# Performance work log

Measured on AMD Instinct MI355X. Metric: run time of the kernel, lower is better.

Reference implementation:

```python
import jax, jax.numpy as jnp
import numpy as np

NEG_SLOPE = 0.1
BN_EPS = 1e-5

def lrelu(z):
    return jax.nn.leaky_relu(z, NEG_SLOPE)

def conv1d(x, w, b):
    # x: [B,C,L], w: [O,I,K], 'same' padding for K=3
    y = jax.lax.conv_general_dilated(x, w, (1,), [(1, 1)], dimension_numbers=('NCH', 'OIH', 'NCH'))
    return y + b[None, :, None]

def batchnorm_train(x, g, be):
    # training-mode BatchNorm1d over (B, L) per channel; x: [B,C,L]
    m = x.mean(axis=(0, 2), keepdims=True)
    v = x.var(axis=(0, 2), keepdims=True)
    return g[None, :, None] * (x - m) * jax.lax.rsqrt(v + BN_EPS) + be[None, :, None]

def setup_inputs() -> dict:
    key = jax.random.key(0)
    ks = jax.random.split(key, 16)
    L, B, E = 100, 32, 512
    F, K, M, H, DEC = 256, 3, 128, 512, 512
    D = F + 2  # cnn feats + 2 coord dims
    s = 0.02
    inp = {
        'x': jax.random.normal(ks[0], (L, B, E), jnp.float32),
        'h': jax.random.normal(ks[1], (B, H), jnp.float32),
        'cw1': jax.random.normal(ks[2], (F, E, K), jnp.float32) * s,
        'cb1': jnp.zeros((F,), jnp.float32),
        'g1': jnp.ones((F,), jnp.float32), 'be1': jnp.zeros((F,), jnp.float32),
        'cw2': jax.random.normal(ks[3], (F, F, K), jnp.float32) * s,
        'cb2': jnp.zeros((F,), jnp.float32),
        'g2': jnp.ones((F,), jnp.float32), 'be2': jnp.zeros((F,), jnp.float32),
        'cw3': jax.random.normal(ks[4], (F, F, K), jnp.float32) * s,
        'cb3': jnp.zeros((F,), jnp.float32),
        'g3': jnp.ones((F,), jnp.float32), 'be3': jnp.zeros((F,), jnp.float32),
        'cw4': jax.random.normal(ks[5], (F, F, K), jnp.float32) * s,
        'cb4': jnp.zeros((F,), jnp.float32),
        'g4': jnp.ones((F,), jnp.float32), 'be4': jnp.zeros((F,), jnp.float32),
        'W1': jax.random.normal(ks[6], (2 * D + H, M), jnp.float32) * s,
        'b1': jnp.zeros((M,), jnp.float32),
        'W2': jax.random.normal(ks[7], (M, M), jnp.float32) * s,
        'b2': jnp.zeros((M,), jnp.float32),
        'W3': jax.random.normal(ks[8], (M, M), jnp.float32) * s,
        'b3': jnp.zeros((M,), jnp.float32),
        'W4': jax.random.normal(ks[9], (M, M), jnp.float32) * s,
        'b4': jnp.zeros((M,), jnp.float32),
        'F1': jax.random.normal(ks[10], (M, M), jnp.float32) * s,
        'fb1': jnp.zeros((M,), jnp.float32),
        'F2': jax.random.normal(ks[11], (M, DEC), jnp.float32) * s,
        'fb2': jnp.zeros((DEC,), jnp.float32),
    }
    return inp

def reference(x, h, cw1, cb1, g1, be1, cw2, cb2, g2, be2, cw3, cb3, g3, be3,
              cw4, cb4, g4, be4, W1, b1, W2, b2, W3, b3, W4, b4, F1, fb1, F2, fb2):
    # x: [L,B,E] -> [B,E,L]
    xc = jnp.transpose(x, (1, 2, 0))
    for cw, cb, g, be in ((cw1, cb1, g1, be1), (cw2, cb2, g2, be2),
                          (cw3, cb3, g3, be3), (cw4, cb4, g4, be4)):
        xc = batchnorm_train(lrelu(conv1d(xc, cw, cb)), g, be)
    xc = jnp.transpose(xc, (0, 2, 1))  # [B,L,F]
    B, L, _ = xc.shape
    # coordinate tensor: cvt_coord(i, L) = [(i/sqrt(L)-2)/2, (i%sqrt(L)-2)/2]
    i = jnp.arange(L, dtype=jnp.float32)
    sL = jnp.sqrt(jnp.float32(L))
    coord = jnp.stack([(i / sL - 2.0) / 2.0, (jnp.mod(i, sL) - 2.0) / 2.0], axis=-1)
    xf = jnp.concatenate([xc, jnp.broadcast_to(coord, (B, L, 2))], axis=-1)  # [B,L,D]
    D = xf.shape[-1]
    # pair[b,i,j] = [xf[b,j], xf[b,i], h[b]]; split W1 to avoid materializing concat
    Wa, Wb, Wc = W1[:D], W1[D:2 * D], W1[2 * D:]
    A = xf @ Wa                              # contribution of x_j, [B,L,M]
    C = xf @ Wb + (h @ Wc + b1)[:, None, :]  # contribution of x_i and h, [B,L,M]
    g = lrelu(C[:, :, None, :] + A[:, None, :, :])  # [B,L,L,M]
    g = lrelu(g @ W2 + b2)
    g = lrelu(g @ W3 + b3)
    g = lrelu(g @ W4 + b4)
    s = g.sum(axis=(1, 2))  # sum-pool over all L*L pairs -> [B,M]
    out = lrelu(lrelu(s @ F1 + fb1) @ F2 + fb2)  # [B,dec_hid]
    return out
```

## Files before the change

### kernel.cpp

```cpp
#include <hip/hip_runtime.h>
#include <hip/hip_bf16.h>
#include <stdint.h>
#include <stddef.h>

#define NEG 0.1f

typedef __attribute__((ext_vector_type(8))) short short8;
typedef __attribute__((ext_vector_type(16))) float floatx16;

__device__ __forceinline__ unsigned f2bf(float f) {
  union { float f; unsigned u; } v; v.f = f;
  unsigned r = v.u + 0x7FFFu + ((v.u >> 16) & 1u);
  return r >> 16;
}
__device__ __forceinline__ unsigned pk2bf(float a, float b) {
  __hip_bfloat162 hh = __float22bfloat162_rn(make_float2(a, b));
  union { __hip_bfloat162 h; unsigned u; } v; v.h = hh; return v.u;
}
__device__ __forceinline__ float bits2f(unsigned u) {
  union { unsigned u; float f; } v; v.u = u; return v.f;
}

__global__ void k_prep(const float* __restrict__ cw1, const float* __restrict__ cw2,
                       const float* __restrict__ cw3, const float* __restrict__ cw4,
                       unsigned short* __restrict__ wt1, unsigned short* __restrict__ wt2,
                       unsigned short* __restrict__ wt3, unsigned short* __restrict__ wt4,
                       const float* __restrict__ W1, unsigned short* __restrict__ wab,
                       const float* __restrict__ W2, const float* __restrict__ W3,
                       const float* __restrict__ W4, unsigned short* __restrict__ wmlp,
                       const float* __restrict__ h, float* __restrict__ hc) {
  __shared__ float tile[64 * 65];
  int bid = blockIdx.x, tid = threadIdx.x;
  if (bid < 1280) {
    int z = bid;
    int E; const float* cw; unsigned short* wt;
    if (z < 512) { E = 512; cw = cw1; wt = wt1; }
    else {
      int q = (z - 512) >> 8; E = 256;
      cw = (q == 0) ? cw2 : ((q == 1) ? cw3 : cw4);
      wt = (q == 0) ? wt2 : ((q == 1) ? wt3 : wt4);
      z = (z - 512) & 255;
    }
    int idx = z * 256 + tid;
    int f = idx / E, e = idx - f * E;
    const float* s = cw + (size_t)idx * 3;
    unsigned short* d = wt + (size_t)f * 3 * E + e;
    d[0] = (unsigned short)f2bf(s[0]);
    d[E] = (unsigned short)f2bf(s[1]);
    d[2 * E] = (unsigned short)f2bf(s[2]);
  } else if (bid < 1304) {
    int tw = bid - 1280;
    int half = tw / 12, rem = tw % 12, dt = rem >> 1, nt = rem & 1;
    int c = tid & 63, rq = tid >> 6;
#pragma unroll
    for (int it = 0; it < 16; ++it) {
      int r = rq + it * 4;
      int kp = dt * 64 + r;
      float v = 0.f;
      if (kp < 258) v = W1[(size_t)(half * 258 + kp) * 128 + nt * 64 + c];
      tile[r * 65 + c] = v;
    }
    __syncthreads();
#pragma unroll
    for (int it = 0; it < 16; ++it) {
      int r2 = rq + it * 4;
      wab[(size_t)(half * 128 + nt * 64 + r2) * 384 + dt * 64 + c] =
          (unsigned short)f2bf(tile[c * 65 + r2]);
    }
  } else if (bid < 1496) {
    int i2 = (bid - 1304) * 256 + tid;
    int n = i2 & 127, k = (i2 >> 7) & 127, zz = i2 >> 14;
    const float* W = (zz == 0) ? W2 : ((zz == 1) ? W3 : W4);
    float v = W[k * 128 + n];
    int w = n >> 5, l = ((k >> 3) & 1) * 32 + (n & 31), kk = k >> 4, j = k & 7;
    int i = (((zz * 4 + w) * 8 + kk) << 9) | (l << 3) | j;
    wmlp[i] = (unsigned short)f2bf(v);
  } else {
    int t = bid - 1496;
    int b = t >> 2, seg = t & 3;
    int m = tid & 127, sub = tid >> 7;
    int k0 = seg * 128 + sub * 64;
    const float* hr = h + b * 512 + k0;
    const float* Wc = W1 + (size_t)(516 + k0) * 128 + m;
    float a0 = 0.f, a1 = 0.f, a2 = 0.f, a3 = 0.f, a4 = 0.f, a5 = 0.f, a6 = 0.f, a7 = 0.f;
#pragma unroll
    for (int k = 0; k < 64; k += 8) {
      a0 += hr[k + 0] * Wc[(size_t)(k + 0) * 128];
      a1 += hr[k + 1] * Wc[(size_t)(k + 1) * 128];
      a2 += hr[k + 2] * Wc[(size_t)(k + 2) * 128];
      a3 += hr[k + 3] * Wc[(size_t)(k + 3) * 128];
      a4 += hr[k + 4] * Wc[(size_t)(k + 4) * 128];
      a5 += hr[k + 5] * Wc[(size_t)(k + 5) * 128];
      a6 += hr[k + 6] * Wc[(size_t)(k + 6) * 128];
      a7 += hr[k + 7] * Wc[(size_t)(k + 7) * 128];
    }
    float s = ((a0 + a1) + (a2 + a3)) + ((a4 + a5) + (a6 + a7));
    atomicAdd(&hc[b * 128 + m], s);
  }
}

__global__ __launch_bounds__(256, 2) void k_conv(
    const float* __restrict__ zin, const float* __restrict__ bnin,
    const float* __restrict__ gamv, const float* __restrict__ betv,
    const unsigned short* __restrict__ wt, const float* __restrict__ cb,
    float* __restrict__ zout, float* __restrict__ bnout, int E, int xmode) {
  extern __shared__ unsigned short smem[];
  const int SL = (E == 512) ? 520 : 264;
  unsigned short* slab = smem;
  unsigned short* Bs = smem + 34 * SL;
  const int K = 3 * E, NC = K >> 6, NCH = NC >> 1;
  const int esh = (E == 512) ? 9 : 8;
  int tid = threadIdx.x;
  int lane = tid & 63, wave = tid >> 6;
  int khalf = wave >> 1, cwave = wave & 1;
  int r0 = blockIdx.x * 32, ct = blockIdx.y;
  int i32 = lane & 31;
  int koff = (lane >> 5) << 3;

  int lrow = (r0 + i32) % 100;
  bool vks0 = (lrow >= 1), vks2 = (lrow <= 98);

  if (xmode) {
    for (int s = wave; s < 34; s += 4) {
      int m = r0 - 1 + s; m = min(max(m, 0), 3199);
      int b = m / 100, l = m - b * 100;
      size_t base = (size_t)(l * 32 + b) * 512;
#pragma unroll
      for (int cc = 0; cc < 2; ++cc) {
        int ch = cc * 256 + lane * 4;
        float4 v = *(const float4*)(zin + base + ch);
        uint2 p; p.x = pk2bf(v.x, v.y); p.y = pk2bf(v.z, v.w);
        *(uint2*)(&slab[s * SL + ch]) = p;
      }
    }
  } else {
    const float inv = 1.f / 3200.f;
    float sc[4], sh[4];
#pragma unroll
    for (int q = 0; q < 4; ++q) {
      int ch = lane * 4 + q;
      float mme = bnin[ch] * inv;
      float var = bnin[256 + ch] * inv - mme * mme;
      sc[q] = gamv[ch] * rsqrtf(var + 1e-5f);
      sh[q] = betv[ch] - mme * sc[q];
    }
    for (int s = wave; s < 34; s += 4) {
      int m = r0 - 1 + s; m = min(max(m, 0), 3199);
      float4 v = *(const float4*)(zin + (size_t)m * 256 + lane * 4);
      uint2 p;
      p.x = pk2bf(v.x * sc[0] + sh[0], v.y * sc[1] + sh[1]);
      p.y = pk2bf(v.z * sc[2] + sh[2], v.w * sc[3] + sh[3]);
      *(uint2*)(&slab[s * SL + lane * 4]) = p;
    }
  }

  floatx16 acc;
#pragma unroll
  for (int q = 0; q < 16; ++q) acc[q] = 0.f;

  int t128 = tid & 127;
  int brow = t128 >> 1, bhalf = (t128 & 1) * 32;
  const unsigned short* wrow = wt + (size_t)(ct * 64 + brow) * K + khalf * NCH * 64 + bhalf;
  uint4 pre[4];
#pragma unroll
  for (int t = 0; t < 4; ++t) pre[t] = *(const uint4*)(wrow + t * 8);

  for (int c = 0; c < NCH; ++c) {
    unsigned short* Bc = Bs + (khalf * 2 + (c & 1)) * (64 * 72);
#pragma unroll
    for (int t = 0; t < 4; ++t)
      *(uint4*)(&Bc[brow * 72 + bhalf + t * 8]) = pre[t];
    __syncthreads();
    if (c + 1 < NCH) {
#pragma unroll
      for (int t = 0; t < 4; ++t)
        pre[t] = *(const uint4*)(wrow + (c + 1) * 64 + t * 8);
    }
    int cg = khalf * NCH + c;
    int ks = (cg << 6) >> esh;
    int ebase = (cg << 6) & (E - 1);
    bool v = (ks == 0) ? vks0 : ((ks == 2) ? vks2 : true);
    int srow = i32 + ks;
#pragma unroll
    for (int kk = 0; kk < 4; ++kk) {
      short8 a = {};
      if (v) a = *(const short8*)(&slab[srow * SL + ebase + kk * 16 + koff]);
      short8 b8 = *(const short8*)(&Bc[(cwave * 32 + i32) * 72 + kk * 16 + koff]);
      acc = __builtin_amdgcn_mfma_f32_32x32x16_bf16(a, b8, acc, 0, 0, 0);
    }
  }

  __syncthreads();
  float* scr = (float*)smem;
  if (khalf == 1) {
#pragma unroll
    for (int reg = 0; reg < 16; ++reg) {
      int rowp = (reg & 3) + 8 * (reg >> 2) + 4 * (lane >> 5);
      scr[cwave * 1024 + rowp * 32 + i32] = acc[reg];
    }
  }
  __syncthreads();
  if (khalf == 0) {
    int f = ct * 64 + cwave * 32 + i32;
    float bias = cb[f];
    float s1 = 0.f, s2 = 0.f;
#pragma unroll
    for (int reg = 0; reg < 16; ++reg) {
      int rowp = (reg & 3) + 8 * (reg >> 2) + 4 * (lane >> 5);
      int m = r0 + rowp;
      float v = acc[reg] + scr[cwave * 1024 + rowp * 32 + i32] + bias;
      v = fmaxf(v, NEG * v);
      zout[(size_t)m * 256 + f] = v;
      s1 += v; s2 += v * v;
    }
    s1 += __shfl_xor(s1, 32, 64);
    s2 += __shfl_xor(s2, 32, 64);
    if (lane < 32) { atomicAdd(&bnout[f], s1); atomicAdd(&bnout[256 + f], s2); }
  }
}

__global__ __launch_bounds__(128, 2) void k_ac(
    const float* __restrict__ zin, const float* __restrict__ bnin,
    const float* __restrict__ gamv, const float* __restrict__ betv,
    const unsigned short* __restrict__ wab, const float* __restrict__ hc,
    const float* __restrict__ b1v,
    unsigned short* __restrict__ Abf, unsigned short* __restrict__ Cbf) {
  __shared__ unsigned short slab[32 * 328];
  __shared__ unsigned short Bs[2 * 64 * 72];
  int tid = threadIdx.x;
  int lane = tid & 63, wave = tid >> 6;
  int r0 = blockIdx.x * 32, ct = blockIdx.y;
  int i32 = lane & 31;
  int koff = (lane >> 5) << 3;
  const float inv = 1.f / 3200.f;

  {
    float sc[4], sh[4];
#pragma unroll
    for (int q = 0; q < 4; ++q) {
      int ch = lane * 4 + q;
      float mme = bnin[ch] * inv;
      float var = bnin[256 + ch] * inv - mme * mme;
      sc[q] = gamv[ch] * rsqrtf(var + 1e-5f);
      sh[q] = betv[ch] - mme * sc[q];
    }
    for (int s = wave; s < 32; s += 2) {
      int m = r0 + s;
      float4 v = *(const float4*)(zin + (size_t)m * 256 + lane * 4);
      uint2 p;
      p.x = pk2bf(v.x * sc[0] + sh[0], v.y * sc[1] + sh[1]);
      p.y = pk2bf(v.z * sc[2] + sh[2], v.w * sc[3] + sh[3]);
      *(uint2*)(&slab[s * 328 + lane * 4]) = p;
    }
    if (wave == 0) {
      int s = i32, half = (lane >> 5) * 32;
      int m = r0 + s, l = m % 100;
      float c0 = ((float)l * 0.1f - 2.0f) * 0.5f;
      float c1 = ((float)(l % 10) - 2.0f) * 0.5f;
#pragma unroll
      for (int seg = 0; seg < 4; ++seg) {
        uint4 z4; z4.x = z4.y = z4.z = z4.w = 0u;
        if (half == 0 && seg == 0) z4.x = pk2bf(c0, c1);
        *(uint4*)(&slab[s * 328 + 256 + half + seg * 8]) = z4;
      }
    }
  }

  floatx16 acc;
#pragma unroll
  for (int q = 0; q < 16; ++q) acc[q] = 0.f;

  int brow = tid >> 1, bhalf = (tid & 1) * 32;
  uint4 pre[4];
#pragma unroll
  for (int t = 0; t < 4; ++t)
    pre[t] = *(const uint4*)(wab + (size_t)(ct * 64 + brow) * 384 + bhalf + t * 8);

  for (int c = 0; c < 5; ++c) {
    unsigned short* Bc = Bs + (c & 1) * (64 * 72);
#pragma unroll
    for (int t = 0; t < 4; ++t)
      *(uint4*)(&Bc[brow * 72 + bhalf + t * 8]) = pre[t];
    __syncthreads();
    if (c + 1 < 5) {
#pragma unroll
      for (int t = 0; t < 4; ++t)
        pre[t] = *(const uint4*)(wab + (size_t)(ct * 64 + brow) * 384 + (c + 1) * 64 + bhalf + t * 8);
    }
#pragma unroll
    for (int kk = 0; kk < 4; ++kk) {
      short8 a = *(const short8*)(&slab[i32 * 328 + c * 64 + kk * 16 + koff]);
      short8 b8 = *(const short8*)(&Bc[(wave * 32 + i32) * 72 + kk * 16 + koff]);
      acc = __builtin_amdgcn_mfma_f32_32x32x16_bf16(a, b8, acc, 0, 0, 0);
    }
  }

  int n = ct * 64 + wave * 32 + i32;
#pragma unroll
  for (int reg = 0; reg < 16; ++reg) {
    int rowp = (reg & 3) + 8 * (reg >> 2) + 4 * (lane >> 5);
    int m = r0 + rowp;
    float v = acc[reg];
    if (ct < 2) {
      Abf[(size_t)m * 128 + n] = (unsigned short)f2bf(v);
    } else {
      int b = m / 100;
      int nc = n - 128;
      Cbf[(size_t)m * 128 + nc] =
          (unsigned short)f2bf(v + hc[b * 128 + nc] + b1v[nc]);
    }
  }
}

__device__ __forceinline__ void mlp_layer(const int z, const unsigned short* wlds,
                                          const float* bias_lds, const int lane,
                                          const int h, const short8 (&gin)[8],
                                          short8 (&gout)[8]) {
#pragma unroll
  for (int a = 0; a < 4; ++a) {
    floatx16 acc;
#pragma unroll
    for (int q = 0; q < 16; ++q) acc[q] = 0.f;
#pragma unroll
    for (int kk = 0; kk < 8; ++kk) {
      short8 wf = *(const short8*)(wlds + (((z * 4 + a) * 8 + kk) << 9) + lane * 8);
      acc = __builtin_amdgcn_mfma_f32_32x32x16_bf16(wf, gin[kk], acc, 0, 0, 0);
    }
#pragma unroll
    for (int qg = 0; qg < 4; ++qg) {
      float4 bb = *(const float4*)(bias_lds + z * 128 + a * 32 + qg * 8 + h * 4);
      float v0 = acc[qg * 4 + 0] + bb.x;
      float v1 = acc[qg * 4 + 1] + bb.y;
      float v2 = acc[qg * 4 + 2] + bb.z;
      float v3 = acc[qg * 4 + 3] + bb.w;
      acc[qg * 4 + 0] = fmaxf(v0, NEG * v0);
      acc[qg * 4 + 1] = fmaxf(v1, NEG * v1);
      acc[qg * 4 + 2] = fmaxf(v2, NEG * v2);
      acc[qg * 4 + 3] = fmaxf(v3, NEG * v3);
    }
#pragma unroll
    for (int c = 0; c < 2; ++c) {
      unsigned X0 = pk2bf(acc[8 * c + 0], acc[8 * c + 1]);
      unsigned X1 = pk2bf(acc[8 * c + 2], acc[8 * c + 3]);
      unsigned Y0 = pk2bf(acc[8 * c + 4], acc[8 * c + 5]);
      unsigned Y1 = pk2bf(acc[8 * c + 6], acc[8 * c + 7]);
      auto p0 = __builtin_amdgcn_permlane32_swap(X0, Y0, false, false);
      auto p1 = __builtin_amdgcn_permlane32_swap(X1, Y1, false, false);
      union { unsigned w[4]; short8 s; } uu;
      uu.w[0] = (unsigned)p0[0]; uu.w[1] = (unsigned)p1[0];
      uu.w[2] = (unsigned)p0[1]; uu.w[3] = (unsigned)p1[1];
      gout[2 * a + c] = uu.s;
    }
  }
}

__global__ __launch_bounds__(1024, 4) void k_mlp(
    const unsigned short* __restrict__ Abf, const unsigned short* __restrict__ Cbf,
    const unsigned short* __restrict__ wmlp, const float* __restrict__ b2,
    const float* __restrict__ b3, const float* __restrict__ b4,
    float* __restrict__ sout) {
  extern __shared__ unsigned short wsm[];
  float* bias_lds = (float*)(wsm + 49152);
  int tid = threadIdx.x, lane = tid & 63, wave = tid >> 6;
  int ln31 = lane & 31, h = lane >> 5;

  {
    const uint4* s4 = (const uint4*)wmlp;
    uint4* d4 = (uint4*)wsm;
#pragma unroll
    for (int i = 0; i < 6; ++i) d4[tid + i * 1024] = s4[tid + i * 1024];
    if (tid < 256) bias_lds[tid] = (tid < 128) ? b2[tid] : b3[tid - 128];
  }
  float b4v[4];
#pragma unroll
  for (int a = 0; a < 4; ++a) b4v[a] = b4[a * 32 + ln31];
  __syncthreads();

  int slot = blockIdx.x * 16 + wave;
  for (int it = 0; it < 3; ++it) {
    int u = it * 4096 + slot;
    if (u >= 10016) break;
    int b = u / 313, lu = u - b * 313;
    int r = lu * 32 + ln31;
    int rc = min(r, 9999);
    int i = rc / 100, j = rc - i * 100;
    const unsigned short* Crow = Cbf + (size_t)(b * 100 + i) * 128 + h * 8;
    const unsigned short* Arow = Abf + (size_t)(b * 100 + j) * 128 + h * 8;

    short8 ga[8], gb[8];
#pragma unroll
    for (int kk = 0; kk < 8; ++kk) {
      uint4 c4 = *(const uint4*)(Crow + kk * 16);
      uint4 a4 = *(const uint4*)(Arow + kk * 16);
      unsigned cw[4] = {c4.x, c4.y, c4.z, c4.w};
      unsigned aw[4] = {a4.x, a4.y, a4.z, a4.w};
      unsigned ow[4];
#pragma unroll
      for (int q = 0; q < 4; ++q) {
        float x0 = bits2f(cw[q] << 16) + bits2f(aw[q] << 16);
        float x1 = bits2f(cw[q] & 0xFFFF0000u) + bits2f(aw[q] & 0xFFFF0000u);
        x0 = fmaxf(x0, NEG * x0);
        x1 = fmaxf(x1, NEG * x1);
        ow[q] = pk2bf(x0, x1);
      }
      union { unsigned w[4]; short8 s; } uu;
      uu.w[0] = ow[0]; uu.w[1] = ow[1]; uu.w[2] = ow[2]; uu.w[3] = ow[3];
      ga[kk] = uu.s;
    }

    mlp_layer(0, wsm, bias_lds, lane, h, ga, gb);
    mlp_layer(1, wsm, bias_lds, lane, h, gb, ga);

#pragma unroll
    for (int a = 0; a < 4; ++a) {
      floatx16 acc;
#pragma unroll
      for (int q = 0; q < 16; ++q) acc[q] = 0.f;
#pragma unroll
      for (int kk = 0; kk < 8; ++kk) {
        short8 wf = *(const short8*)(wsm + (((8 + a) * 8 + kk) << 9) + lane * 8);
        acc = __builtin_amdgcn_mfma_f32_32x32x16_bf16(ga[kk], wf, acc, 0, 0, 0);
      }
      float s = 0.f;
#pragma unroll
      for (int reg = 0; reg < 16; ++reg) {
        int rowp = (reg & 3) + 8 * (reg >> 2) + 4 * h;
        float v = acc[reg] + b4v[a];
        v = fmaxf(v, NEG * v);
        s += (lu * 32 + rowp < 10000) ? v : 0.f;
      }
      s += __shfl_xor(s, 32, 64);
      if (lane < 32) atomicAdd(&sout[b * 128 + a * 32 + ln31], s);
    }
  }
}

__global__ void k_final(const float* __restrict__ s, const float* __restrict__ F1,
                        const float* __restrict__ fb1, const float* __restrict__ F2,
                        const float* __restrict__ fb2, float* __restrict__ out) {
  __shared__ float sl[128], t1[128];
  int b = blockIdx.x, t = threadIdx.x;
  if (t < 128) sl[t] = s[b * 128 + t];
  __syncthreads();
  if (t < 128) {
    float a = fb1[t];
    for (int k = 0; k < 128; ++k) a += sl[k] * F1[k * 128 + t];
    t1[t] = fmaxf(a, NEG * a);
  }
  __syncthreads();
  for (int o = t; o < 512; o += 256) {
    float a = fb2[o];
    for (int k = 0; k < 128; ++k) a += t1[k] * F2[k * 512 + o];
    out[b * 512 + o] = fmaxf(a, NEG * a);
  }
}

extern "C" void kernel_launch(void* const* d_in, const int* in_sizes, int n_in,
                              void* d_out, int out_size, void* d_ws, size_t ws_size,
                              hipStream_t stream) {
  const float* x   = (const float*)d_in[0];
  const float* h   = (const float*)d_in[1];
  const float* cw1 = (const float*)d_in[2];
  const float* cb1 = (const float*)d_in[3];
  const float* g1  = (const float*)d_in[4];
  const float* be1 = (const float*)d_in[5];
  const float* cw2 = (const float*)d_in[6];
  const float* cb2 = (const float*)d_in[7];
  const float* g2  = (const float*)d_in[8];
  const float* be2 = (const float*)d_in[9];
  const float* cw3 = (const float*)d_in[10];
  const float* cb3 = (const float*)d_in[11];
  const float* g3  = (const float*)d_in[12];
  const float* be3 = (const float*)d_in[13];
  const float* cw4 = (const float*)d_in[14];
  const float* cb4 = (const float*)d_in[15];
  const float* g4  = (const float*)d_in[16];
  const float* be4 = (const float*)d_in[17];
  const float* W1  = (const float*)d_in[18];
  const float* b1  = (const float*)d_in[19];
  const float* W2  = (const float*)d_in[20];
  const float* b2  = (const float*)d_in[21];
  const float* W3  = (const float*)d_in[22];
  const float* b3  = (const float*)d_in[23];
  const float* W4  = (const float*)d_in[24];
  const float* b4  = (const float*)d_in[25];
  const float* F1  = (const float*)d_in[26];
  const float* fb1 = (const float*)d_in[27];
  const float* F2  = (const float*)d_in[28];
  const float* fb2 = (const float*)d_in[29];

  char* ws = (char*)d_ws;
  float* bn0  = (float*)(ws + 0);
  float* bn1  = (float*)(ws + 2048);
  float* bn2  = (float*)(ws + 4096);
  float* bn3  = (float*)(ws + 6144);
  float* sbuf = (float*)(ws + 8192);
  float* hc   = (float*)(ws + 24576);
  float* za   = (float*)(ws + 40960);
  float* zb   = (float*)(ws + 3317760);
  unsigned short* wt1  = (unsigned short*)(ws + 6594560);
  unsigned short* wt2  = (unsigned short*)(ws + 7380992);
  unsigned short* wt3  = (unsigned short*)(ws + 7774208);
  unsigned short* wt4  = (unsigned short*)(ws + 8167424);
  unsigned short* wab  = (unsigned short*)(ws + 8560640);
  unsigned short* wmlp = (unsigned short*)(ws + 8757248);
  unsigned short* Abf  = (unsigned short*)(ws + 8855552);
  unsigned short* Cbf  = (unsigned short*)(ws + 9674752);

  hipMemsetAsync(d_ws, 0, 40960, stream);

  k_prep<<<1624, 256, 0, stream>>>(cw1, cw2, cw3, cw4, wt1, wt2, wt3, wt4,
                                   W1, wab, W2, W3, W4, wmlp, h, hc);

  const int lds1 = (34 * 520 + 4 * 64 * 72) * 2;
  const int lds2 = (34 * 264 + 4 * 64 * 72) * 2;
  k_conv<<<dim3(100, 4), 256, lds1, stream>>>(x,  nullptr, nullptr, nullptr, wt1, cb1, za, bn0, 512, 1);
  k_conv<<<dim3(100, 4), 256, lds2, stream>>>(za, bn0, g1, be1, wt2, cb2, zb, bn1, 256, 0);
  k_conv<<<dim3(100, 4), 256, lds2, stream>>>(zb, bn1, g2, be2, wt3, cb3, za, bn2, 256, 0);
  k_conv<<<dim3(100, 4), 256, lds2, stream>>>(za, bn2, g3, be3, wt4, cb4, zb, bn3, 256, 0);

  k_ac<<<dim3(100, 4), 128, 0, stream>>>(zb, bn3, g4, be4, wab, hc, b1, Abf, Cbf);

  const int ldsm = 49152 * 2 + 256 * 4;
  k_mlp<<<256, 1024, ldsm, stream>>>(Abf, Cbf, wmlp, b2, b3, b4, sbuf);
  k_final<<<32, 256, 0, stream>>>(sbuf, F1, fb1, F2, fb2, (float*)d_out);
}
```

Baseline: 280.8 us.

## Fuse conv stack and projection into cooperative kernel with grid syncs

Replaces four conv launches and the projection launch with one cooperative kernel that uses grid-wide syncs between phases. It also folds the final MLP into k_mlp after a grid sync, and replaces the memset with zeroing blocks in k_prep. The projection now splits K across four waves and reduces through LDS, and biases are folded into the MFMA accumulator init, with the masking branch kept only for the tail. This removes launch and memset gaps, but cooperative launch requires all blocks to be co-resident and each grid sync adds its own cost.

```diff
diff --git a/kernel.cpp b/kernel.cpp
--- a/kernel.cpp
+++ b/kernel.cpp
@@ -1,7 +1,10 @@
 #include <hip/hip_runtime.h>
+#include <hip/hip_cooperative_groups.h>
 #include <hip/hip_bf16.h>
 #include <stdint.h>
 #include <stddef.h>
+
+namespace cg = cooperative_groups;
 
 #define NEG 0.1f
 
@@ -28,7 +31,8 @@
                        const float* __restrict__ W1, unsigned short* __restrict__ wab,
                        const float* __restrict__ W2, const float* __restrict__ W3,
                        const float* __restrict__ W4, unsigned short* __restrict__ wmlp,
-                       const float* __restrict__ h, float* __restrict__ hc) {
+                       const float* __restrict__ h, float* __restrict__ hc,
+                       float* __restrict__ zmem) {
   __shared__ float tile[64 * 65];
   int bid = blockIdx.x, tid = threadIdx.x;
   if (bid < 1280) {
@@ -75,16 +79,14 @@
     int w = n >> 5, l = ((k >> 3) & 1) * 32 + (n & 31), kk = k >> 4, j = k & 7;
     int i = (((zz * 4 + w) * 8 + kk) << 9) | (l << 3) | j;
     wmlp[i] = (unsigned short)f2bf(v);
-  } else {
-    int t = bid - 1496;
-    int b = t >> 2, seg = t & 3;
-    int m = tid & 127, sub = tid >> 7;
-    int k0 = seg * 128 + sub * 64;
-    const float* hr = h + b * 512 + k0;
-    const float* Wc = W1 + (size_t)(516 + k0) * 128 + m;
+  } else if (bid < 1528) {
+    int b = bid - 1496;
+    int m = tid & 127, kh = tid >> 7;
+    const float* hr = h + b * 512 + kh * 256;
+    const float* Wc = W1 + (size_t)(516 + kh * 256) * 128 + m;
     float a0 = 0.f, a1 = 0.f, a2 = 0.f, a3 = 0.f, a4 = 0.f, a5 = 0.f, a6 = 0.f, a7 = 0.f;
 #pragma unroll
-    for (int k = 0; k < 64; k += 8) {
+    for (int k = 0; k < 256; k += 8) {
       a0 += hr[k + 0] * Wc[(size_t)(k + 0) * 128];
       a1 += hr[k + 1] * Wc[(size_t)(k + 1) * 128];
       a2 += hr[k + 2] * Wc[(size_t)(k + 2) * 128];
@@ -95,16 +97,19 @@
       a7 += hr[k + 7] * Wc[(size_t)(k + 7) * 128];
     }
     float s = ((a0 + a1) + (a2 + a3)) + ((a4 + a5) + (a6 + a7));
-    atomicAdd(&hc[b * 128 + m], s);
-  }
-}
-
-__global__ __launch_bounds__(256, 2) void k_conv(
-    const float* __restrict__ zin, const float* __restrict__ bnin,
-    const float* __restrict__ gamv, const float* __restrict__ betv,
-    const unsigned short* __restrict__ wt, const float* __restrict__ cb,
-    float* __restrict__ zout, float* __restrict__ bnout, int E, int xmode) {
-  extern __shared__ unsigned short smem[];
+    tile[tid] = s;
+    __syncthreads();
+    if (kh == 0) hc[b * 128 + m] = tile[m] + tile[128 + m];
+  } else {
+    int i = (bid - 1528) * 256 + tid;
+    zmem[i] = 0.f;
+  }
+}
+
+__device__ void conv_phase(unsigned short* smem,
+    const float* zin, const float* bnin, const float* gamv, const float* betv,
+    const unsigned short* wt, const float* cb,
+    float* zout, float* bnout, int E, int xmode) {
   const int SL = (E == 512) ? 520 : 264;
   unsigned short* slab = smem;
   unsigned short* Bs = smem + 34 * SL;
@@ -113,7 +118,8 @@
   int tid = threadIdx.x;
   int lane = tid & 63, wave = tid >> 6;
   int khalf = wave >> 1, cwave = wave & 1;
-  int r0 = blockIdx.x * 32, ct = blockIdx.y;
+  int bid = blockIdx.x;
+  int r0 = (bid % 100) * 32, ct = bid / 100;
   int i32 = lane & 31;
   int koff = (lane >> 5) << 3;
 
@@ -219,17 +225,17 @@
   }
 }
 
-__global__ __launch_bounds__(128, 2) void k_ac(
-    const float* __restrict__ zin, const float* __restrict__ bnin,
-    const float* __restrict__ gamv, const float* __restrict__ betv,
-    const unsigned short* __restrict__ wab, const float* __restrict__ hc,
-    const float* __restrict__ b1v,
-    unsigned short* __restrict__ Abf, unsigned short* __restrict__ Cbf) {
-  __shared__ unsigned short slab[32 * 328];
-  __shared__ unsigned short Bs[2 * 64 * 72];
+__device__ void ac_phase(unsigned short* smem,
+    const float* zin, const float* bnin, const float* gamv, const float* betv,
+    const unsigned short* wab, const float* hc, const float* b1v,
+    unsigned short* Abf, unsigned short* Cbf) {
+  unsigned short* slab = smem;
+  unsigned short* Bs = smem + 32 * 328;
   int tid = threadIdx.x;
   int lane = tid & 63, wave = tid >> 6;
-  int r0 = blockIdx.x * 32, ct = blockIdx.y;
+  int khalf = wave >> 1, cwave = wave & 1;
+  int bid = blockIdx.x;
+  int r0 = (bid % 100) * 32, ct = bid / 100;
   int i32 = lane & 31;
   int koff = (lane >> 5) << 3;
   const float inv = 1.f / 3200.f;
@@ -244,7 +250,7 @@
       sc[q] = gamv[ch] * rsqrtf(var + 1e-5f);
       sh[q] = betv[ch] - mme * sc[q];
     }
-    for (int s = wave; s < 32; s += 2) {
+    for (int s = wave; s < 32; s += 4) {
       int m = r0 + s;
       float4 v = *(const float4*)(zin + (size_t)m * 256 + lane * 4);
       uint2 p;
@@ -270,46 +276,88 @@
 #pragma unroll
   for (int q = 0; q < 16; ++q) acc[q] = 0.f;
 
-  int brow = tid >> 1, bhalf = (tid & 1) * 32;
+  int t128 = tid & 127;
+  int brow = t128 >> 1, bhalf = (t128 & 1) * 32;
+  const unsigned short* wrow = wab + (size_t)(ct * 64 + brow) * 384 + khalf * 128 + bhalf;
+  const int NCH = khalf ? 3 : 2;
   uint4 pre[4];
 #pragma unroll
-  for (int t = 0; t < 4; ++t)
-    pre[t] = *(const uint4*)(wab + (size_t)(ct * 64 + brow) * 384 + bhalf + t * 8);
-
-  for (int c = 0; c < 5; ++c) {
-    unsigned short* Bc = Bs + (c & 1) * (64 * 72);
-#pragma unroll
-    for (int t = 0; t < 4; ++t)
-      *(uint4*)(&Bc[brow * 72 + bhalf + t * 8]) = pre[t];
+  for (int t = 0; t < 4; ++t) pre[t] = *(const uint4*)(wrow + t * 8);
+
+  for (int c = 0; c < 3; ++c) {
+    unsigned short* Bc = Bs + (khalf * 2 + (c & 1)) * (64 * 72);
+    if (c < NCH) {
+#pragma unroll
+      for (int t = 0; t < 4; ++t)
+        *(uint4*)(&Bc[brow * 72 + bhalf + t * 8]) = pre[t];
+    }
     __syncthreads();
-    if (c + 1 < 5) {
+    if (c + 1 < NCH) {
 #pragma unroll
       for (int t = 0; t < 4; ++t)
-        pre[t] = *(const uint4*)(wab + (size_t)(ct * 64 + brow) * 384 + (c + 1) * 64 + bhalf + t * 8);
-    }
-#pragma unroll
-    for (int kk = 0; kk < 4; ++kk) {
-      short8 a = *(const short8*)(&slab[i32 * 328 + c * 64 + kk * 16 + koff]);
-      short8 b8 = *(const short8*)(&Bc[(wave * 32 + i32) * 72 + kk * 16 + koff]);
-      acc = __builtin_amdgcn_mfma_f32_32x32x16_bf16(a, b8, acc, 0, 0, 0);
-    }
-  }
-
-  int n = ct * 64 + wave * 32 + i32;
-#pragma unroll
-  for (int reg = 0; reg < 16; ++reg) {
-    int rowp = (reg & 3) + 8 * (reg >> 2) + 4 * (lane >> 5);
-    int m = r0 + rowp;
-    float v = acc[reg];
-    if (ct < 2) {
-      Abf[(size_t)m * 128 + n] = (unsigned short)f2bf(v);
-    } else {
-      int b = m / 100;
-      int nc = n - 128;
-      Cbf[(size_t)m * 128 + nc] =
-          (unsigned short)f2bf(v + hc[b * 128 + nc] + b1v[nc]);
-    }
-  }
+        pre[t] = *(const uint4*)(wrow + (c + 1) * 64 + t * 8);
+    }
+    if (c < NCH) {
+      int chunk = khalf * 2 + c;
+#pragma unroll
+      for (int kk = 0; kk < 4; ++kk) {
+        short8 a = *(const short8*)(&slab[i32 * 328 + chunk * 64 + kk * 16 + koff]);
+        short8 b8 = *(const short8*)(&Bc[(cwave * 32 + i32) * 72 + kk * 16 + koff]);
+        acc = __builtin_amdgcn_mfma_f32_32x32x16_bf16(a, b8, acc, 0, 0, 0);
+      }
+    }
+  }
+
+  __syncthreads();
+  float* scr = (float*)smem;
+  if (khalf == 1) {
+#pragma unroll
+    for (int reg = 0; reg < 16; ++reg) {
+      int rowp = (reg & 3) + 8 * (reg >> 2) + 4 * (lane >> 5);
+      scr[cwave * 1024 + rowp * 32 + i32] = acc[reg];
+    }
+  }
+  __syncthreads();
+  if (khalf == 0) {
+    int n = ct * 64 + cwave * 32 + i32;
+#pragma unroll
+    for (int reg = 0; reg < 16; ++reg) {
+      int rowp = (reg & 3) + 8 * (reg >> 2) + 4 * (lane >> 5);
+      int m = r0 + rowp;
+      float v = acc[reg] + scr[cwave * 1024 + rowp * 32 + i32];
+      if (ct < 2) {
+        Abf[(size_t)m * 128 + n] = (unsigned short)f2bf(v);
+      } else {
+        int b = m / 100;
+        int nc = n - 128;
+        Cbf[(size_t)m * 128 + nc] =
+            (unsigned short)f2bf(v + hc[b * 128 + nc] + b1v[nc]);
+      }
+    }
+  }
+}
+
+__global__ __launch_bounds__(256, 2) void k_net(
+    const float* x, float* za, float* zb,
+    float* bn0, float* bn1, float* bn2, float* bn3,
+    const float* g1, const float* be1, const float* g2, const float* be2,
+    const float* g3, const float* be3, const float* g4, const float* be4,
+    const unsigned short* wt1, const unsigned short* wt2,
+    const unsigned short* wt3, const unsigned short* wt4,
+    const float* cb1, const float* cb2, const float* cb3, const float* cb4,
+    const unsigned short* wab, const float* hc, const float* b1v,
+    unsigned short* Abf, unsigned short* Cbf) {
+  extern __shared__ unsigned short smem[];
+  cg::grid_group grid = cg::this_grid();
+  conv_phase(smem, x,  nullptr, nullptr, nullptr, wt1, cb1, za, bn0, 512, 1);
+  grid.sync();
+  conv_phase(smem, za, bn0, g1, be1, wt2, cb2, zb, bn1, 256, 0);
+  grid.sync();
+  conv_phase(smem, zb, bn1, g2, be2, wt3, cb3, za, bn2, 256, 0);
+  grid.sync();
+  conv_phase(smem, za, bn2, g3, be3, wt4, cb4, zb, bn3, 256, 0);
+  grid.sync();
+  ac_phase(smem, zb, bn3, g4, be4, wab, hc, b1v, Abf, Cbf);
 }
 
 __device__ __forceinline__ void mlp_layer(const int z, const unsigned short* wlds,
@@ -320,23 +368,20 @@
   for (int a = 0; a < 4; ++a) {
     floatx16 acc;
 #pragma unroll
-    for (int q = 0; q < 16; ++q) acc[q] = 0.f;
+    for (int qg = 0; qg < 4; ++qg) {
+      float4 bb = *(const float4*)(bias_lds + z * 128 + a * 32 + qg * 8 + h * 4);
+      acc[qg * 4 + 0] = bb.x; acc[qg * 4 + 1] = bb.y;
+      acc[qg * 4 + 2] = bb.z; acc[qg * 4 + 3] = bb.w;
+    }
 #pragma unroll
     for (int kk = 0; kk < 8; ++kk) {
       short8 wf = *(const short8*)(wlds + (((z * 4 + a) * 8 + kk) << 9) + lane * 8);
       acc = __builtin_amdgcn_mfma_f32_32x32x16_bf16(wf, gin[kk], acc, 0, 0, 0);
     }
 #pragma unroll
-    for (int qg = 0; qg < 4; ++qg) {
-      float4 bb = *(const float4*)(bias_lds + z * 128 + a * 32 + qg * 8 + h * 4);
-      float v0 = acc[qg * 4 + 0] + bb.x;
-      float v1 = acc[qg * 4 + 1] + bb.y;
-      float v2 = acc[qg * 4 + 2] + bb.z;
-      float v3 = acc[qg * 4 + 3] + bb.w;
-      acc[qg * 4 + 0] = fmaxf(v0, NEG * v0);
-      acc[qg * 4 + 1] = fmaxf(v1, NEG * v1);
-      acc[qg * 4 + 2] = fmaxf(v2, NEG * v2);
-      acc[qg * 4 + 3] = fmaxf(v3, NEG * v3);
+    for (int q = 0; q < 16; ++q) {
+      float v = acc[q];
+      acc[q] = fmaxf(v, NEG * v);
     }
 #pragma unroll
     for (int c = 0; c < 2; ++c) {
@@ -355,10 +400,11 @@
 }
 
 __global__ __launch_bounds__(1024, 4) void k_mlp(
-    const unsigned short* __restrict__ Abf, const unsigned short* __restrict__ Cbf,
-    const unsigned short* __restrict__ wmlp, const float* __restrict__ b2,
-    const float* __restrict__ b3, const float* __restrict__ b4,
-    float* __restrict__ sout) {
+    const unsigned short* Abf, const unsigned short* Cbf,
+    const unsigned short* wmlp, const float* b2, const float* b3,
+    const float* b4, float* sout,
+    const float* F1, const float* fb1, const float* F2, const float* fb2,
+    float* out) {
   extern __shared__ unsigned short wsm[];
   float* bias_lds = (float*)(wsm + 49152);
   int tid = threadIdx.x, lane = tid & 63, wave = tid >> 6;
@@ -381,8 +427,9 @@
     int u = it * 4096 + slot;
     if (u >= 10016) break;
     int b = u / 313, lu = u - b * 313;
+    bool tail = (lu == 312);
     int r = lu * 32 + ln31;
-    int rc = min(r, 9999);
+    int rc = tail ? min(r, 9999) : r;
     int i = rc / 100, j = rc - i * 100;
     const unsigned short* Crow = Cbf + (size_t)(b * 100 + i) * 128 + h * 8;
     const unsigned short* Arow = Abf + (size_t)(b * 100 + j) * 128 + h * 8;
@@ -414,44 +461,53 @@
 #pragma unroll
     for (int a = 0; a < 4; ++a) {
       floatx16 acc;
-#pragma unroll
-      for (int q = 0; q < 16; ++q) acc[q] = 0.f;
+      float binit = b4v[a];
+#pragma unroll
+      for (int q = 0; q < 16; ++q) acc[q] = binit;
 #pragma unroll
       for (int kk = 0; kk < 8; ++kk) {
         short8 wf = *(const short8*)(wsm + (((8 + a) * 8 + kk) << 9) + lane * 8);
         acc = __builtin_amdgcn_mfma_f32_32x32x16_bf16(ga[kk], wf, acc, 0, 0, 0);
       }
       float s = 0.f;
-#pragma unroll
-      for (int reg = 0; reg < 16; ++reg) {
-        int rowp = (reg & 3) + 8 * (reg >> 2) + 4 * h;
-        float v = acc[reg] + b4v[a];
-        v = fmaxf(v, NEG * v);
-        s += (lu * 32 + rowp < 10000) ? v : 0.f;
+      if (!tail) {
+#pragma unroll
+        for (int reg = 0; reg < 16; ++reg) {
+          float v = acc[reg];
+          s += fmaxf(v, NEG * v);
+        }
+      } else {
+#pragma unroll
+        for (int reg = 0; reg < 16; ++reg) {
+          int rowp = (reg & 3) + 8 * (reg >> 2) + 4 * h;
+          float v = acc[reg];
+          v = fmaxf(v, NEG * v);
+          s += (lu * 32 + rowp < 10000) ? v : 0.f;
+        }
       }
       s += __shfl_xor(s, 32, 64);
       if (lane < 32) atomicAdd(&sout[b * 128 + a * 32 + ln31], s);
     }
   }
-}
-
-__global__ void k_final(const float* __restrict__ s, const float* __restrict__ F1,
-                        const float* __restrict__ fb1, const float* __restrict__ F2,
-                        const float* __restrict__ fb2, float* __restrict__ out) {
-  __shared__ float sl[128], t1[128];
-  int b = blockIdx.x, t = threadIdx.x;
-  if (t < 128) sl[t] = s[b * 128 + t];
-  __syncthreads();
-  if (t < 128) {
-    float a = fb1[t];
-    for (int k = 0; k < 128; ++k) a += sl[k] * F1[k * 128 + t];
-    t1[t] = fmaxf(a, NEG * a);
-  }
-  __syncthreads();
-  for (int o = t; o < 512; o += 256) {
-    float a = fb2[o];
-    for (int k = 0; k < 128; ++k) a += t1[k] * F2[k * 512 + o];
-    out[b * 512 + o] = fmaxf(a, NEG * a);
+
+  cg::this_grid().sync();
+
+  if (blockIdx.x < 32) {
+    int b = blockIdx.x, t = threadIdx.x;
+    float* fs = (float*)wsm;
+    if (t < 128) fs[t] = sout[b * 128 + t];
+    __syncthreads();
+    if (t < 128) {
+      float a = fb1[t];
+      for (int k = 0; k < 128; ++k) a += fs[k] * F1[k * 128 + t];
+      fs[128 + t] = fmaxf(a, NEG * a);
+    }
+    __syncthreads();
+    if (t < 512) {
+      float a = fb2[t];
+      for (int k = 0; k < 128; ++k) a += fs[128 + k] * F2[k * 512 + t];
+      out[b * 512 + t] = fmaxf(a, NEG * a);
+    }
   }
 }
 
@@ -490,6 +546,7 @@
   const float* fb2 = (const float*)d_in[29];
 
   char* ws = (char*)d_ws;
+  float* zmem = (float*)(ws + 0);
   float* bn0  = (float*)(ws + 0);
   float* bn1  = (float*)(ws + 2048);
   float* bn2  = (float*)(ws + 4096);
@@ -507,21 +564,34 @@
   unsigned short* Abf  = (unsigned short*)(ws + 8855552);
   unsigned short* Cbf  = (unsigned short*)(ws + 9674752);
 
-  hipMemsetAsync(d_ws, 0, 40960, stream);
-
-  k_prep<<<1624, 256, 0, stream>>>(cw1, cw2, cw3, cw4, wt1, wt2, wt3, wt4,
-                                   W1, wab, W2, W3, W4, wmlp, h, hc);
+  k_prep<<<1552, 256, 0, stream>>>(cw1, cw2, cw3, cw4, wt1, wt2, wt3, wt4,
+                                   W1, wab, W2, W3, W4, wmlp, h, hc, zmem);
 
   const int lds1 = (34 * 520 + 4 * 64 * 72) * 2;
-  const int lds2 = (34 * 264 + 4 * 64 * 72) * 2;
-  k_conv<<<dim3(100, 4), 256, lds1, stream>>>(x,  nullptr, nullptr, nullptr, wt1, cb1, za, bn0, 512, 1);
-  k_conv<<<dim3(100, 4), 256, lds2, stream>>>(za, bn0, g1, be1, wt2, cb2, zb, bn1, 256, 0);
-  k_conv<<<dim3(100, 4), 256, lds2, stream>>>(zb, bn1, g2, be2, wt3, cb3, za, bn2, 256, 0);
-  k_conv<<<dim3(100, 4), 256, lds2, stream>>>(za, bn2, g3, be3, wt4, cb4, zb, bn3, 256, 0);
-
-  k_ac<<<dim3(100, 4), 128, 0, stream>>>(zb, bn3, g4, be4, wab, hc, b1, Abf, Cbf);
+  {
+    void* args[] = {
+      (void*)&x, (void*)&za, (void*)&zb,
+      (void*)&bn0, (void*)&bn1, (void*)&bn2, (void*)&bn3,
+      (void*)&g1, (void*)&be1, (void*)&g2, (void*)&be2,
+      (void*)&g3, (void*)&be3, (void*)&g4, (void*)&be4,
+      (void*)&wt1, (void*)&wt2, (void*)&wt3, (void*)&wt4,
+      (void*)&cb1, (void*)&cb2, (void*)&cb3, (void*)&cb4,
+      (void*)&wab, (void*)&hc, (void*)&b1,
+      (void*)&Abf, (void*)&Cbf
+    };
+    hipLaunchCooperativeKernel(k_net, dim3(400), dim3(256), args,
+                               (unsigned int)lds1, stream);
+  }
 
   const int ldsm = 49152 * 2 + 256 * 4;
-  k_mlp<<<256, 1024, ldsm, stream>>>(Abf, Cbf, wmlp, b2, b3, b4, sbuf);
-  k_final<<<32, 256, 0, stream>>>(sbuf, F1, fb1, F2, fb2, (float*)d_out);
-}
+  {
+    float* outp = (float*)d_out;
+    void* args[] = {
+      (void*)&Abf, (void*)&Cbf, (void*)&wmlp, (void*)&b2, (void*)&b3,
+      (void*)&b4, (void*)&sbuf,
+      (void*)&F1, (void*)&fb1, (void*)&F2, (void*)&fb2, (void*)&outp
+    };
+    hipLaunchCooperativeKernel(k_mlp, dim3(256), dim3(1024), args,
+                               (unsigned int)ldsm, stream);
+  }
+}
```

New measurement: 517.3 us. 1.84x slower.
